# Performance work log

Measured on AMD Instinct MI355X. Metric: run time of the kernel, lower is better.

The kernel has to match this reference:

```python
import jax, jax.numpy as jnp
import numpy as np

PATCH = (2, 4, 4)
WIN = 4
SHIFT = 2
NLAYERS = 16  # depth=8 -> 8 (no-shift, shift) pairs interleaved
PD = 32       # patch_dim = 2*4*4
D_MAIN = 64   # patch_dim * 2
NHEAD = 2
HEAD_DIM = D_MAIN // NHEAD
FFN = 2
EPS = 1.1920929e-07  # torch.finfo(float32).eps (nn.RMSNorm default eps=None)


def rms_norm(x, w):
    return x * jax.lax.rsqrt(jnp.mean(x * x, axis=-1, keepdims=True) + EPS) * w


def _attn_mask(grid):
    # standard Swin shifted-window mask, built statically with numpy
    Dg, Hg, Wg = grid
    w, s = WIN, SHIFT
    img = np.zeros(grid, np.int32)
    cnt = 0
    sl = (slice(0, -w), slice(-w, -s), slice(-s, None))
    for a in sl:
        for b in sl:
            for c in sl:
                img[a, b, c] = cnt
                cnt += 1
    m = img.reshape(Dg // w, w, Hg // w, w, Wg // w, w)
    m = m.transpose(0, 2, 4, 1, 3, 5).reshape(-1, w ** 3)  # (nW, N)
    mask = np.where(m[:, None, :] != m[:, :, None], -100.0, 0.0).astype(np.float32)
    return jnp.asarray(mask)  # (nW, N, N)


def _window_partition(x, w):
    # (B, Dg, Hg, Wg, C) -> (B*nW, w^3, C)
    B, Dg, Hg, Wg, C = x.shape
    x = x.reshape(B, Dg // w, w, Hg // w, w, Wg // w, w, C)
    return x.transpose(0, 1, 3, 5, 2, 4, 6, 7).reshape(-1, w ** 3, C)


def _window_reverse(x, w, B, Dg, Hg, Wg):
    C = x.shape[-1]
    x = x.reshape(B, Dg // w, Hg // w, Wg // w, w, w, w, C)
    return x.transpose(0, 1, 4, 2, 5, 3, 6, 7).reshape(B, Dg, Hg, Wg, C)


def _swin_layer(x, grid, shift, mask, ln1, qkv_w, proj_w, proj_b, ln2, w1, b1, w2, b2):
    B, L, C = x.shape
    Dg, Hg, Wg = grid
    N = WIN ** 3
    shortcut = x
    h = rms_norm(x, ln1).reshape(B, Dg, Hg, Wg, C)
    if shift:
        h = jnp.roll(h, (-shift, -shift, -shift), axis=(1, 2, 3))
    hw = _window_partition(h, WIN)  # (Bw, N, C)
    Bw = hw.shape[0]
    qkv = (hw @ qkv_w).reshape(Bw, N, 3, NHEAD, HEAD_DIM)
    q, k, v = qkv[:, :, 0], qkv[:, :, 1], qkv[:, :, 2]  # (Bw, N, nh, hd)
    attn = jnp.einsum('bnhd,bmhd->bhnm', q, k) * (HEAD_DIM ** -0.5)
    if mask is not None:
        nW = mask.shape[0]
        attn = (attn.reshape(B, nW, NHEAD, N, N) + mask[None, :, None]).reshape(Bw, NHEAD, N, N)
    attn = jax.nn.softmax(attn, axis=-1)
    out = jnp.einsum('bhnm,bmhd->bnhd', attn, v).reshape(Bw, N, C)
    out = out @ proj_w + proj_b
    h = _window_reverse(out, WIN, B, Dg, Hg, Wg)
    if shift:
        h = jnp.roll(h, (shift, shift, shift), axis=(1, 2, 3))
    x = shortcut + h.reshape(B, L, C)
    h = rms_norm(x, ln2)
    h = jax.nn.gelu(h @ w1 + b1, approximate=False) @ w2 + b2
    return x + h


def setup_inputs() -> dict:
    key = jax.random.key(0)
    ks = jax.random.split(key, 10)
    def w(k, shape):
        return (jax.random.normal(k, shape, jnp.float32) * 0.02)
    B, D, H, W = 1, 64, 256, 256
    return {
        'x': jax.random.normal(ks[0], (B, 1, D, H, W), jnp.float32),
        'up_w': w(ks[1], (PD, D_MAIN)), 'up_b': jnp.zeros((D_MAIN,), jnp.float32),
        'ln1_w': jnp.ones((NLAYERS, D_MAIN), jnp.float32),
        'qkv_w': w(ks[2], (NLAYERS, D_MAIN, 3 * D_MAIN)),
        'proj_w': w(ks[3], (NLAYERS, D_MAIN, D_MAIN)),
        'proj_b': jnp.zeros((NLAYERS, D_MAIN), jnp.float32),
        'ln2_w': jnp.ones((NLAYERS, D_MAIN), jnp.float32),
        'mlp_w1': w(ks[4], (NLAYERS, D_MAIN, FFN * D_MAIN)),
        'mlp_b1': jnp.zeros((NLAYERS, FFN * D_MAIN), jnp.float32),
        'mlp_w2': w(ks[5], (NLAYERS, FFN * D_MAIN, D_MAIN)),
        'mlp_b2': jnp.zeros((NLAYERS, D_MAIN), jnp.float32),
        'down_p_w': w(ks[6], (D_MAIN, PD)), 'down_p_b': jnp.zeros((PD,), jnp.float32),
        'down_c_w': w(ks[7], (D_MAIN, PD)), 'down_c_b': jnp.zeros((PD,), jnp.float32),
    }


def reference(x, up_w, up_b, ln1_w, qkv_w, proj_w, proj_b, ln2_w,
              mlp_w1, mlp_b1, mlp_w2, mlp_b2, down_p_w, down_p_b, down_c_w, down_c_b):
    B, C, D, H, W = x.shape
    pd, ph, pw = PATCH
    Dg, Hg, Wg = D // pd, H // ph, W // pw
    L = Dg * Hg * Wg
    # unfoldNd (kernel == stride): non-overlapping patch extraction
    t = x.reshape(B, Dg, pd, Hg, ph, Wg, pw)
    t = t.transpose(0, 1, 3, 5, 2, 4, 6).reshape(B, L, PD)
    h = t @ up_w + up_b  # (B, L, 64)
    mask = _attn_mask((Dg, Hg, Wg))
    for i in range(NLAYERS):
        shift = SHIFT if (i % 2 == 1) else 0
        h = _swin_layer(h, (Dg, Hg, Wg), shift, mask if shift else None,
                        ln1_w[i], qkv_w[i], proj_w[i], proj_b[i], ln2_w[i],
                        mlp_w1[i], mlp_b1[i], mlp_w2[i], mlp_b2[i])
    p = h @ down_p_w + down_p_b
    c = h @ down_c_w + down_c_b
    def fold(t):
        t = t.reshape(B, Dg, Hg, Wg, pd, ph, pw)
        return t.transpose(0, 1, 4, 2, 5, 3, 6).reshape(B, 1, D, H, W)
    return (fold(p), fold(c))
```

## Files before the change

kernel.cpp:

```cpp
#include <hip/hip_runtime.h>
#include <hip/hip_bf16.h>


#define EPSV 1.1920929e-07f
#define QSW 196
#define HAW 72
#define HA_LO (64*72)
#define HTW 136
#define HT_LO (64*136)

typedef short short8 __attribute__((ext_vector_type(8)));
typedef float f32x4 __attribute__((ext_vector_type(4)));

#define MFMA3(d, ah_, al_, bh_, bl_)                                     \
    d = __builtin_amdgcn_mfma_f32_16x16x32_bf16(ah_, bh_, d, 0, 0, 0);   \
    d = __builtin_amdgcn_mfma_f32_16x16x32_bf16(ah_, bl_, d, 0, 0, 0);   \
    d = __builtin_amdgcn_mfma_f32_16x16x32_bf16(al_, bh_, d, 0, 0, 0);

__device__ __forceinline__ void split2(float v, short& hs, short& ls) {
    unsigned u = __float_as_uint(v);
    float hf = __uint_as_float(u & 0xFFFF0000u);
    float lf = v - hf;
    hs = (short)(u >> 16);
    ls = (short)(__float_as_uint(lf) >> 16);
}

__global__ __launch_bounds__(256) void k_embed(const float* __restrict__ x,
        const float* __restrict__ up_w, const float* __restrict__ up_b,
        float* __restrict__ h) {
    int t = blockIdx.x * 256 + threadIdx.x;
    int tok = t >> 2, seg = t & 3;
    int xg = tok & 63, yg = (tok >> 6) & 63, zg = tok >> 12;
    const float* xp = x + ((size_t)(zg * 2) * 256 + yg * 4) * 256 + xg * 4;
    float p[32];
    #pragma unroll
    for (int dz = 0; dz < 2; ++dz)
        #pragma unroll
        for (int dy = 0; dy < 4; ++dy) {
            float4 v = *reinterpret_cast<const float4*>(xp + ((size_t)dz * 256 + dy) * 256);
            int b = (dz * 4 + dy) * 4;
            p[b] = v.x; p[b + 1] = v.y; p[b + 2] = v.z; p[b + 3] = v.w;
        }
    float acc[16];
    #pragma unroll
    for (int j = 0; j < 16; ++j) acc[j] = up_b[seg * 16 + j];
    #pragma unroll
    for (int k = 0; k < 32; ++k) {
        float a = p[k];
        const float* wr = up_w + k * 64 + seg * 16;
        #pragma unroll
        for (int j = 0; j < 16; ++j) acc[j] = fmaf(a, wr[j], acc[j]);
    }
    float* op = h + (size_t)tok * 64 + seg * 16;
    #pragma unroll
    for (int j = 0; j < 16; ++j) op[j] = acc[j];
}

template <int SHIFTED>
__global__ __launch_bounds__(256, 2) void k_layer(float* __restrict__ h,
        const float* __restrict__ ln1, const float* __restrict__ qkvw,
        const float* __restrict__ projw, const float* __restrict__ projb,
        const float* __restrict__ ln2, const float* __restrict__ w1,
        const float* __restrict__ b1, const float* __restrict__ w2,
        const float* __restrict__ b2) {
    __shared__ __align__(16) unsigned short hA[2 * 64 * HAW];
    __shared__ __align__(16) float qs[64 * QSW];
    __shared__ int rid_s[64];

    float* hAf = (float*)hA;
    unsigned short* ht_hi = (unsigned short*)qs;
    unsigned short* ht_lo = (unsigned short*)qs + HT_LO;

    int w = blockIdx.x;
    int wx = w & 15, wy = (w >> 4) & 15, wz = w >> 8;
    int tid = threadIdx.x;
    int tok = tid >> 2, seg = tid & 3;
    int wv = tid >> 6, lane = tid & 63, lr = lane & 15, lg = lane >> 4;

    float v[16];
    int lidx;

    {
        int nz = tok >> 4, ny = (tok >> 2) & 3, nx = tok & 3;
        int gz = wz * 4 + nz, gy = wy * 4 + ny, gx = wx * 4 + nx;
        int sz, sy, sx;
        if (SHIFTED) { sz = (gz + 2) & 31; sy = (gy + 2) & 63; sx = (gx + 2) & 63; }
        else         { sz = gz; sy = gy; sx = gx; }
        lidx = (sz * 64 + sy) * 64 + sx;
        if (SHIFTED && seg == 0) {
            int rz = gz >= 30 ? 2 : (gz >= 28 ? 1 : 0);
            int ry = gy >= 62 ? 2 : (gy >= 60 ? 1 : 0);
            int rx = gx >= 62 ? 2 : (gx >= 60 ? 1 : 0);
            rid_s[tok] = rz * 9 + ry * 3 + rx;
        }
        const float* hp = h + (size_t)lidx * 64 + seg * 16;
        #pragma unroll
        for (int c = 0; c < 4; ++c) {
            float4 t4 = *reinterpret_cast<const float4*>(hp + c * 4);
            v[c * 4] = t4.x; v[c * 4 + 1] = t4.y; v[c * 4 + 2] = t4.z; v[c * 4 + 3] = t4.w;
        }
        float ss = 0.f;
        #pragma unroll
        for (int j = 0; j < 16; ++j) ss = fmaf(v[j], v[j], ss);
        ss += __shfl_xor(ss, 1);
        ss += __shfl_xor(ss, 2);
        float r = rsqrtf(ss * (1.0f / 64.0f) + EPSV);
        short8 sh[2], sl[2];
        #pragma unroll
        for (int j = 0; j < 16; ++j) {
            float nv = v[j] * r * ln1[seg * 16 + j];
            short hs, ls; split2(nv, hs, ls);
            sh[j >> 3][j & 7] = hs; sl[j >> 3][j & 7] = ls;
        }
        *reinterpret_cast<short8*>(&hA[tok * HAW + seg * 16])         = sh[0];
        *reinterpret_cast<short8*>(&hA[tok * HAW + seg * 16 + 8])     = sh[1];
        *reinterpret_cast<short8*>(&hA[HA_LO + tok * HAW + seg * 16])     = sl[0];
        *reinterpret_cast<short8*>(&hA[HA_LO + tok * HAW + seg * 16 + 8]) = sl[1];
    }
    __syncthreads();

    {
        short8 ah[4][2], al[4][2];
        #pragma unroll
        for (int mt = 0; mt < 4; ++mt)
            #pragma unroll
            for (int ks = 0; ks < 2; ++ks) {
                int off = (mt * 16 + lr) * HAW + ks * 32 + lg * 8;
                ah[mt][ks] = *reinterpret_cast<const short8*>(&hA[off]);
                al[mt][ks] = *reinterpret_cast<const short8*>(&hA[HA_LO + off]);
            }
        #pragma unroll
        for (int nt = 0; nt < 3; ++nt) {
            int c0 = wv * 48 + nt * 16;
            short8 bh[2], bl[2];
            #pragma unroll
            for (int ks = 0; ks < 2; ++ks) {
                const float* p = qkvw + (size_t)(ks * 32 + lg * 8) * 192 + c0 + lr;
                #pragma unroll
                for (int e = 0; e < 8; ++e) {
                    short hs, ls; split2(p[e * 192], hs, ls);
                    bh[ks][e] = hs; bl[ks][e] = ls;
                }
            }
            f32x4 acc[4];
            #pragma unroll
            for (int mt = 0; mt < 4; ++mt) acc[mt] = (f32x4)(0.f);
            #pragma unroll
            for (int mt = 0; mt < 4; ++mt)
                #pragma unroll
                for (int ks = 0; ks < 2; ++ks) {
                    MFMA3(acc[mt], ah[mt][ks], al[mt][ks], bh[ks], bl[ks]);
                }
            #pragma unroll
            for (int mt = 0; mt < 4; ++mt)
                #pragma unroll
                for (int j = 0; j < 4; ++j)
                    qs[(mt * 16 + lg * 4 + j) * QSW + c0 + lr] = acc[mt][j];
        }
    }
    __syncthreads();

    {
        int hh = tid >> 7, n = (tid >> 1) & 63, dh = tid & 1;
        int qo = hh * 32 + dh * 16;
        float q[16];
        #pragma unroll
        for (int c = 0; c < 4; ++c) {
            float4 t4 = *reinterpret_cast<const float4*>(&qs[n * QSW + qo + c * 4]);
            q[c * 4] = t4.x; q[c * 4 + 1] = t4.y; q[c * 4 + 2] = t4.z; q[c * 4 + 3] = t4.w;
        }
        float s[64];
        int myrid = SHIFTED ? rid_s[n] : 0;
        const float scale = 0.17677669529663687f;
        #pragma unroll
        for (int m = 0; m < 64; ++m) {
            float a = 0.f;
            #pragma unroll
            for (int c = 0; c < 4; ++c) {
                float4 kv = *reinterpret_cast<const float4*>(&qs[m * QSW + 64 + qo + c * 4]);
                a = fmaf(q[c * 4 + 0], kv.x, a);
                a = fmaf(q[c * 4 + 1], kv.y, a);
                a = fmaf(q[c * 4 + 2], kv.z, a);
                a = fmaf(q[c * 4 + 3], kv.w, a);
            }
            a += __shfl_xor(a, 1);
            a *= scale;
            if (SHIFTED && rid_s[m] != myrid) a -= 100.f;
            s[m] = a;
        }
        float mx = s[0];
        #pragma unroll
        for (int m = 1; m < 64; ++m) mx = fmaxf(mx, s[m]);
        float sum = 0.f;
        #pragma unroll
        for (int m = 0; m < 64; ++m) { float e = __expf(s[m] - mx); s[m] = e; sum += e; }
        float inv = 1.0f / sum;
        float o[16];
        #pragma unroll
        for (int j = 0; j < 16; ++j) o[j] = 0.f;
        #pragma unroll
        for (int m = 0; m < 64; ++m) {
            float p = s[m];
            #pragma unroll
            for (int c = 0; c < 4; ++c) {
                float4 vv = *reinterpret_cast<const float4*>(&qs[m * QSW + 128 + qo + c * 4]);
                o[c * 4 + 0] = fmaf(p, vv.x, o[c * 4 + 0]);
                o[c * 4 + 1] = fmaf(p, vv.y, o[c * 4 + 1]);
                o[c * 4 + 2] = fmaf(p, vv.z, o[c * 4 + 2]);
                o[c * 4 + 3] = fmaf(p, vv.w, o[c * 4 + 3]);
            }
        }
        short8 sh[2], sl[2];
        #pragma unroll
        for (int j = 0; j < 16; ++j) {
            short hs, ls; split2(o[j] * inv, hs, ls);
            sh[j >> 3][j & 7] = hs; sl[j >> 3][j & 7] = ls;
        }
        *reinterpret_cast<short8*>(&hA[n * HAW + qo])             = sh[0];
        *reinterpret_cast<short8*>(&hA[n * HAW + qo + 8])         = sh[1];
        *reinterpret_cast<short8*>(&hA[HA_LO + n * HAW + qo])     = sl[0];
        *reinterpret_cast<short8*>(&hA[HA_LO + n * HAW + qo + 8]) = sl[1];
    }
    __syncthreads();

    {
        short8 ah[4][2], al[4][2];
        #pragma unroll
        for (int mt = 0; mt < 4; ++mt)
            #pragma unroll
            for (int ks = 0; ks < 2; ++ks) {
                int off = (mt * 16 + lr) * HAW + ks * 32 + lg * 8;
                ah[mt][ks] = *reinterpret_cast<const short8*>(&hA[off]);
                al[mt][ks] = *reinterpret_cast<const short8*>(&hA[HA_LO + off]);
            }
        int c0 = wv * 16;
        short8 bh[2], bl[2];
        #pragma unroll
        for (int ks = 0; ks < 2; ++ks) {
            const float* p = projw + (size_t)(ks * 32 + lg * 8) * 64 + c0 + lr;
            #pragma unroll
            for (int e = 0; e < 8; ++e) {
                short hs, ls; split2(p[e * 64], hs, ls);
                bh[ks][e] = hs; bl[ks][e] = ls;
            }
        }
        f32x4 acc[4];
        #pragma unroll
        for (int mt = 0; mt < 4; ++mt) acc[mt] = (f32x4)(0.f);
        #pragma unroll
        for (int mt = 0; mt < 4; ++mt)
            #pragma unroll
            for (int ks = 0; ks < 2; ++ks) {
                MFMA3(acc[mt], ah[mt][ks], al[mt][ks], bh[ks], bl[ks]);
            }
        float pb = projb[c0 + lr];
        #pragma unroll
        for (int mt = 0; mt < 4; ++mt)
            #pragma unroll
            for (int j = 0; j < 4; ++j)
                qs[(mt * 16 + lg * 4 + j) * QSW + c0 + lr] = acc[mt][j] + pb;
    }
    __syncthreads();

    {
        #pragma unroll
        for (int j = 0; j < 16; ++j) v[j] += qs[tok * QSW + seg * 16 + j];
        float ss = 0.f;
        #pragma unroll
        for (int j = 0; j < 16; ++j) ss = fmaf(v[j], v[j], ss);
        ss += __shfl_xor(ss, 1);
        ss += __shfl_xor(ss, 2);
        float r = rsqrtf(ss * (1.0f / 64.0f) + EPSV);
        short8 sh[2], sl[2];
        #pragma unroll
        for (int j = 0; j < 16; ++j) {
            float nv = v[j] * r * ln2[seg * 16 + j];
            short hs, ls; split2(nv, hs, ls);
            sh[j >> 3][j & 7] = hs; sl[j >> 3][j & 7] = ls;
        }
        *reinterpret_cast<short8*>(&hA[tok * HAW + seg * 16])         = sh[0];
        *reinterpret_cast<short8*>(&hA[tok * HAW + seg * 16 + 8])     = sh[1];
        *reinterpret_cast<short8*>(&hA[HA_LO + tok * HAW + seg * 16])     = sl[0];
        *reinterpret_cast<short8*>(&hA[HA_LO + tok * HAW + seg * 16 + 8]) = sl[1];
    }
    __syncthreads();

    {
        short8 ah[4][2], al[4][2];
        #pragma unroll
        for (int mt = 0; mt < 4; ++mt)
            #pragma unroll
            for (int ks = 0; ks < 2; ++ks) {
                int off = (mt * 16 + lr) * HAW + ks * 32 + lg * 8;
                ah[mt][ks] = *reinterpret_cast<const short8*>(&hA[off]);
                al[mt][ks] = *reinterpret_cast<const short8*>(&hA[HA_LO + off]);
            }
        #pragma unroll
        for (int nt = 0; nt < 2; ++nt) {
            int c0 = wv * 32 + nt * 16;
            short8 bh[2], bl[2];
            #pragma unroll
            for (int ks = 0; ks < 2; ++ks) {
                const float* p = w1 + (size_t)(ks * 32 + lg * 8) * 128 + c0 + lr;
                #pragma unroll
                for (int e = 0; e < 8; ++e) {
                    short hs, ls; split2(p[e * 128], hs, ls);
                    bh[ks][e] = hs; bl[ks][e] = ls;
                }
            }
            f32x4 acc[4];
            #pragma unroll
            for (int mt = 0; mt < 4; ++mt) acc[mt] = (f32x4)(0.f);
            #pragma unroll
            for (int mt = 0; mt < 4; ++mt)
                #pragma unroll
                for (int ks = 0; ks < 2; ++ks) {
                    MFMA3(acc[mt], ah[mt][ks], al[mt][ks], bh[ks], bl[ks]);
                }
            float bb = b1[c0 + lr];
            #pragma unroll
            for (int mt = 0; mt < 4; ++mt)
                #pragma unroll
                for (int j = 0; j < 4; ++j) {
                    float u = acc[mt][j] + bb;
                    float g = 0.5f * u * (1.0f + erff(u * 0.70710678118654752f));
                    short hs, ls; split2(g, hs, ls);
                    int off = (mt * 16 + lg * 4 + j) * HTW + c0 + lr;
                    ht_hi[off] = (unsigned short)hs;
                    ht_lo[off] = (unsigned short)ls;
                }
        }
    }
    __syncthreads();

    {
        int c0 = wv * 16;
        f32x4 acc[4];
        #pragma unroll
        for (int mt = 0; mt < 4; ++mt) acc[mt] = (f32x4)(0.f);
        #pragma unroll
        for (int ks = 0; ks < 4; ++ks) {
            short8 bh, bl;
            const float* p = w2 + (size_t)(ks * 32 + lg * 8) * 64 + c0 + lr;
            #pragma unroll
            for (int e = 0; e < 8; ++e) {
                short hs, ls; split2(p[e * 64], hs, ls);
                bh[e] = hs; bl[e] = ls;
            }
            #pragma unroll
            for (int mt = 0; mt < 4; ++mt) {
                int off = (mt * 16 + lr) * HTW + ks * 32 + lg * 8;
                short8 ah = *reinterpret_cast<const short8*>(&ht_hi[off]);
                short8 al = *reinterpret_cast<const short8*>(&ht_lo[off]);
                MFMA3(acc[mt], ah, al, bh, bl);
            }
        }
        __syncthreads();
        float bb = b2[c0 + lr];
        #pragma unroll
        for (int mt = 0; mt < 4; ++mt)
            #pragma unroll
            for (int j = 0; j < 4; ++j)
                hAf[(mt * 16 + lg * 4 + j) * HAW + c0 + lr] = acc[mt][j] + bb;
    }
    __syncthreads();

    {
        float* op = h + (size_t)lidx * 64 + seg * 16;
        #pragma unroll
        for (int c = 0; c < 4; ++c) {
            float4 o4;
            o4.x = v[c * 4 + 0] + hAf[tok * HAW + seg * 16 + c * 4 + 0];
            o4.y = v[c * 4 + 1] + hAf[tok * HAW + seg * 16 + c * 4 + 1];
            o4.z = v[c * 4 + 2] + hAf[tok * HAW + seg * 16 + c * 4 + 2];
            o4.w = v[c * 4 + 3] + hAf[tok * HAW + seg * 16 + c * 4 + 3];
            *reinterpret_cast<float4*>(op + c * 4) = o4;
        }
    }
}

__global__ __launch_bounds__(256) void k_down(const float* __restrict__ h,
        const float* __restrict__ wp, const float* __restrict__ bp,
        const float* __restrict__ wc, const float* __restrict__ bc,
        float* __restrict__ out) {
    int t = blockIdx.x * 256 + threadIdx.x;
    int tok = t >> 1, pc = t & 1;
    const float* wsel = pc ? wc : wp;
    const float* bsel = pc ? bc : bp;
    float* obase = out + (size_t)pc * (64u * 256u * 256u);
    float hv[64];
    const float* hp = h + (size_t)tok * 64;
    #pragma unroll
    for (int j4 = 0; j4 < 16; ++j4) {
        float4 t4 = *reinterpret_cast<const float4*>(hp + j4 * 4);
        hv[j4 * 4] = t4.x; hv[j4 * 4 + 1] = t4.y; hv[j4 * 4 + 2] = t4.z; hv[j4 * 4 + 3] = t4.w;
    }
    float acc[32];
    #pragma unroll
    for (int j = 0; j < 32; ++j) acc[j] = bsel[j];
    #pragma unroll 4
    for (int k = 0; k < 64; ++k) {
        float a = hv[k];
        const float* wr = wsel + k * 32;
        #pragma unroll
        for (int j = 0; j < 32; ++j) acc[j] = fmaf(a, wr[j], acc[j]);
    }
    int xg = tok & 63, yg = (tok >> 6) & 63, zg = tok >> 12;
    float* op = obase + ((size_t)(zg * 2) * 256 + yg * 4) * 256 + xg * 4;
    #pragma unroll
    for (int dz = 0; dz < 2; ++dz)
        #pragma unroll
        for (int dy = 0; dy < 4; ++dy) {
            int b = (dz * 4 + dy) * 4;
            *reinterpret_cast<float4*>(op + ((size_t)dz * 256 + dy) * 256) =
                make_float4(acc[b], acc[b + 1], acc[b + 2], acc[b + 3]);
        }
}

extern "C" void kernel_launch(void* const* d_in, const int* in_sizes, int n_in,
                              void* d_out, int out_size, void* d_ws, size_t ws_size,
                              hipStream_t stream) {
    const float* x        = (const float*)d_in[0];
    const float* up_w     = (const float*)d_in[1];
    const float* up_b     = (const float*)d_in[2];
    const float* ln1_w    = (const float*)d_in[3];
    const float* qkv_w    = (const float*)d_in[4];
    const float* proj_w   = (const float*)d_in[5];
    const float* proj_b   = (const float*)d_in[6];
    const float* ln2_w    = (const float*)d_in[7];
    const float* mlp_w1   = (const float*)d_in[8];
    const float* mlp_b1   = (const float*)d_in[9];
    const float* mlp_w2   = (const float*)d_in[10];
    const float* mlp_b2   = (const float*)d_in[11];
    const float* down_p_w = (const float*)d_in[12];
    const float* down_p_b = (const float*)d_in[13];
    const float* down_c_w = (const float*)d_in[14];
    const float* down_c_b = (const float*)d_in[15];
    float* out = (float*)d_out;
    float* h   = (float*)d_ws;

    k_embed<<<2048, 256, 0, stream>>>(x, up_w, up_b, h);
    for (int i = 0; i < 16; ++i) {
        const float* a0 = ln1_w + i * 64;
        const float* a1 = qkv_w  + (size_t)i * 64 * 192;
        const float* a2 = proj_w + (size_t)i * 64 * 64;
        const float* a3 = proj_b + i * 64;
        const float* a4 = ln2_w + i * 64;
        const float* a5 = mlp_w1 + (size_t)i * 64 * 128;
        const float* a6 = mlp_b1 + i * 128;
        const float* a7 = mlp_w2 + (size_t)i * 128 * 64;
        const float* a8 = mlp_b2 + i * 64;
        if (i & 1) k_layer<1><<<2048, 256, 0, stream>>>(h, a0, a1, a2, a3, a4, a5, a6, a7, a8);
        else       k_layer<0><<<2048, 256, 0, stream>>>(h, a0, a1, a2, a3, a4, a5, a6, a7, a8);
    }
    k_down<<<1024, 256, 0, stream>>>(h, down_p_w, down_p_b, down_c_w, down_c_b, out);
}
```

Measured before the change: 1.856 ms.

## Pre-split weights into bf16 hi/lo MFMA fragment layout and restage down-projection

Adds a prologue kernel that splits all per-layer weight matrices once into bf16 hi/lo halves, stored in the exact per-lane MFMA B-fragment order. Each layer kernel then loads whole short8 fragments instead of doing eight strided fp32 gathers plus splits per fragment, in every block. The down-projection kernel is also rewritten so each block stages a row of tokens and both weight matrices in shared memory, computing both outputs per thread with float4 stores. This costs one extra launch and a workspace region at a fixed 32MB offset, which assumes the workspace is large enough.

```diff
diff --git a/kernel.cpp b/kernel.cpp
--- a/kernel.cpp
+++ b/kernel.cpp
@@ -9,6 +9,13 @@
 #define HTW 136
 #define HT_LO (64*136)
 
+#define LAYER_WSZ 32768
+#define WOFF_QKV  0
+#define WOFF_PROJ 12288
+#define WOFF_W1   16384
+#define WOFF_W2   24576
+#define WTOT      (16 * LAYER_WSZ)
+
 typedef short short8 __attribute__((ext_vector_type(8)));
 typedef float f32x4 __attribute__((ext_vector_type(4)));
 
@@ -23,6 +30,30 @@
     float lf = v - hf;
     hs = (short)(u >> 16);
     ls = (short)(__float_as_uint(lf) >> 16);
+}
+
+__global__ __launch_bounds__(256) void k_wsplit(const float* __restrict__ qkv_w,
+        const float* __restrict__ proj_w, const float* __restrict__ w1,
+        const float* __restrict__ w2, unsigned short* __restrict__ wsout) {
+    int t = blockIdx.x * 256 + threadIdx.x;
+    int layer = t >> 15;
+    int r = t & 32767;
+    const float* src; int ncols, idx, nks;
+    if (r < WOFF_PROJ)      { src = qkv_w  + (size_t)layer * 12288; ncols = 192; idx = r;             nks = 2; }
+    else if (r < WOFF_W1)   { src = proj_w + (size_t)layer * 4096;  ncols = 64;  idx = r - WOFF_PROJ; nks = 2; }
+    else if (r < WOFF_W2)   { src = w1     + (size_t)layer * 8192;  ncols = 128; idx = r - WOFF_W1;   nks = 2; }
+    else                    { src = w2     + (size_t)layer * 8192;  ncols = 64;  idx = r - WOFF_W2;   nks = 4; }
+    int e  = idx & 7;
+    int lr = (idx >> 3) & 15;
+    int lg = (idx >> 7) & 3;
+    int q  = idx >> 9;
+    int ks = q & (nks - 1);
+    int ct = q / nks;
+    int k = ks * 32 + lg * 8 + e;
+    int c = ct * 16 + lr;
+    short hs, ls; split2(src[k * ncols + c], hs, ls);
+    wsout[t]        = (unsigned short)hs;
+    wsout[WTOT + t] = (unsigned short)ls;
 }
 
 __global__ __launch_bounds__(256) void k_embed(const float* __restrict__ x,
@@ -58,11 +89,10 @@
 
 template <int SHIFTED>
 __global__ __launch_bounds__(256, 2) void k_layer(float* __restrict__ h,
-        const float* __restrict__ ln1, const float* __restrict__ qkvw,
-        const float* __restrict__ projw, const float* __restrict__ projb,
-        const float* __restrict__ ln2, const float* __restrict__ w1,
-        const float* __restrict__ b1, const float* __restrict__ w2,
-        const float* __restrict__ b2) {
+        const float* __restrict__ ln1,
+        const unsigned short* __restrict__ whi, const unsigned short* __restrict__ wlo,
+        const float* __restrict__ projb, const float* __restrict__ ln2,
+        const float* __restrict__ b1, const float* __restrict__ b2) {
     __shared__ __align__(16) unsigned short hA[2 * 64 * HAW];
     __shared__ __align__(16) float qs[64 * QSW];
     __shared__ int rid_s[64];
@@ -131,16 +161,14 @@
             }
         #pragma unroll
         for (int nt = 0; nt < 3; ++nt) {
-            int c0 = wv * 48 + nt * 16;
+            int ct = wv * 3 + nt;
+            int c0 = ct * 16;
             short8 bh[2], bl[2];
             #pragma unroll
             for (int ks = 0; ks < 2; ++ks) {
-                const float* p = qkvw + (size_t)(ks * 32 + lg * 8) * 192 + c0 + lr;
-                #pragma unroll
-                for (int e = 0; e < 8; ++e) {
-                    short hs, ls; split2(p[e * 192], hs, ls);
-                    bh[ks][e] = hs; bl[ks][e] = ls;
-                }
+                int fo = WOFF_QKV + ((ct * 2 + ks) * 4 + lg) * 128 + lr * 8;
+                bh[ks] = *reinterpret_cast<const short8*>(&whi[fo]);
+                bl[ks] = *reinterpret_cast<const short8*>(&wlo[fo]);
             }
             f32x4 acc[4];
             #pragma unroll
@@ -237,12 +265,9 @@
         short8 bh[2], bl[2];
         #pragma unroll
         for (int ks = 0; ks < 2; ++ks) {
-            const float* p = projw + (size_t)(ks * 32 + lg * 8) * 64 + c0 + lr;
-            #pragma unroll
-            for (int e = 0; e < 8; ++e) {
-                short hs, ls; split2(p[e * 64], hs, ls);
-                bh[ks][e] = hs; bl[ks][e] = ls;
-            }
+            int fo = WOFF_PROJ + ((wv * 2 + ks) * 4 + lg) * 128 + lr * 8;
+            bh[ks] = *reinterpret_cast<const short8*>(&whi[fo]);
+            bl[ks] = *reinterpret_cast<const short8*>(&wlo[fo]);
         }
         f32x4 acc[4];
         #pragma unroll
@@ -297,16 +322,14 @@
             }
         #pragma unroll
         for (int nt = 0; nt < 2; ++nt) {
-            int c0 = wv * 32 + nt * 16;
+            int ct = wv * 2 + nt;
+            int c0 = ct * 16;
             short8 bh[2], bl[2];
             #pragma unroll
             for (int ks = 0; ks < 2; ++ks) {
-                const float* p = w1 + (size_t)(ks * 32 + lg * 8) * 128 + c0 + lr;
-                #pragma unroll
-                for (int e = 0; e < 8; ++e) {
-                    short hs, ls; split2(p[e * 128], hs, ls);
-                    bh[ks][e] = hs; bl[ks][e] = ls;
-                }
+                int fo = WOFF_W1 + ((ct * 2 + ks) * 4 + lg) * 128 + lr * 8;
+                bh[ks] = *reinterpret_cast<const short8*>(&whi[fo]);
+                bl[ks] = *reinterpret_cast<const short8*>(&wlo[fo]);
             }
             f32x4 acc[4];
             #pragma unroll
@@ -340,13 +363,9 @@
         for (int mt = 0; mt < 4; ++mt) acc[mt] = (f32x4)(0.f);
         #pragma unroll
         for (int ks = 0; ks < 4; ++ks) {
-            short8 bh, bl;
-            const float* p = w2 + (size_t)(ks * 32 + lg * 8) * 64 + c0 + lr;
-            #pragma unroll
-            for (int e = 0; e < 8; ++e) {
-                short hs, ls; split2(p[e * 64], hs, ls);
-                bh[e] = hs; bl[e] = ls;
-            }
+            int fo = WOFF_W2 + ((wv * 4 + ks) * 4 + lg) * 128 + lr * 8;
+            short8 bh = *reinterpret_cast<const short8*>(&whi[fo]);
+            short8 bl = *reinterpret_cast<const short8*>(&wlo[fo]);
             #pragma unroll
             for (int mt = 0; mt < 4; ++mt) {
                 int off = (mt * 16 + lr) * HTW + ks * 32 + lg * 8;
@@ -383,37 +402,60 @@
         const float* __restrict__ wp, const float* __restrict__ bp,
         const float* __restrict__ wc, const float* __restrict__ bc,
         float* __restrict__ out) {
-    int t = blockIdx.x * 256 + threadIdx.x;
-    int tok = t >> 1, pc = t & 1;
-    const float* wsel = pc ? wc : wp;
-    const float* bsel = pc ? bc : bp;
-    float* obase = out + (size_t)pc * (64u * 256u * 256u);
+    __shared__ float hs_[64][68];
+    __shared__ float ws_[2][64][32];
+    int b = blockIdx.x;
+    int zg = b >> 6, yg = b & 63;
+    int tid = threadIdx.x;
+    const float* hp = h + (size_t)(zg * 64 + yg) * 64 * 64;
+    for (int i = tid; i < 1024; i += 256) {
+        float4 t4 = reinterpret_cast<const float4*>(hp)[i];
+        int tokx = i >> 4, c4 = (i & 15) * 4;
+        *reinterpret_cast<float4*>(&hs_[tokx][c4]) = t4;
+    }
+    for (int i = tid; i < 512; i += 256) {
+        reinterpret_cast<float4*>(&ws_[0][0][0])[i] = reinterpret_cast<const float4*>(wp)[i];
+        reinterpret_cast<float4*>(&ws_[1][0][0])[i] = reinterpret_cast<const float4*>(wc)[i];
+    }
+    __syncthreads();
+    int dc = tid >> 6, xg = tid & 63;
     float hv[64];
-    const float* hp = h + (size_t)tok * 64;
-    #pragma unroll
-    for (int j4 = 0; j4 < 16; ++j4) {
-        float4 t4 = *reinterpret_cast<const float4*>(hp + j4 * 4);
-        hv[j4 * 4] = t4.x; hv[j4 * 4 + 1] = t4.y; hv[j4 * 4 + 2] = t4.z; hv[j4 * 4 + 3] = t4.w;
-    }
-    float acc[32];
-    #pragma unroll
-    for (int j = 0; j < 32; ++j) acc[j] = bsel[j];
-    #pragma unroll 4
+    #pragma unroll
+    for (int j = 0; j < 16; ++j) {
+        float4 t4 = *reinterpret_cast<const float4*>(&hs_[xg][j * 4]);
+        hv[j * 4] = t4.x; hv[j * 4 + 1] = t4.y; hv[j * 4 + 2] = t4.z; hv[j * 4 + 3] = t4.w;
+    }
+    float4 acc[2][2];
+    #pragma unroll
+    for (int pc = 0; pc < 2; ++pc) {
+        const float* bsel = pc ? bc : bp;
+        #pragma unroll
+        for (int ci = 0; ci < 2; ++ci)
+            acc[pc][ci] = *reinterpret_cast<const float4*>(bsel + (dc + ci * 4) * 4);
+    }
+    #pragma unroll 8
     for (int k = 0; k < 64; ++k) {
         float a = hv[k];
-        const float* wr = wsel + k * 32;
-        #pragma unroll
-        for (int j = 0; j < 32; ++j) acc[j] = fmaf(a, wr[j], acc[j]);
-    }
-    int xg = tok & 63, yg = (tok >> 6) & 63, zg = tok >> 12;
-    float* op = obase + ((size_t)(zg * 2) * 256 + yg * 4) * 256 + xg * 4;
-    #pragma unroll
-    for (int dz = 0; dz < 2; ++dz)
-        #pragma unroll
-        for (int dy = 0; dy < 4; ++dy) {
-            int b = (dz * 4 + dy) * 4;
-            *reinterpret_cast<float4*>(op + ((size_t)dz * 256 + dy) * 256) =
-                make_float4(acc[b], acc[b + 1], acc[b + 2], acc[b + 3]);
+        #pragma unroll
+        for (int pc = 0; pc < 2; ++pc)
+            #pragma unroll
+            for (int ci = 0; ci < 2; ++ci) {
+                float4 w4 = *reinterpret_cast<const float4*>(&ws_[pc][k][(dc + ci * 4) * 4]);
+                acc[pc][ci].x = fmaf(a, w4.x, acc[pc][ci].x);
+                acc[pc][ci].y = fmaf(a, w4.y, acc[pc][ci].y);
+                acc[pc][ci].z = fmaf(a, w4.z, acc[pc][ci].z);
+                acc[pc][ci].w = fmaf(a, w4.w, acc[pc][ci].w);
+            }
+    }
+    #pragma unroll
+    for (int pc = 0; pc < 2; ++pc)
+        #pragma unroll
+        for (int ci = 0; ci < 2; ++ci) {
+            int cb = dc + ci * 4;
+            int dz = cb >> 2, dy = cb & 3;
+            float* op = out + (size_t)pc * (64u * 256u * 256u)
+                      + ((size_t)(zg * 2 + dz) * 256 + (yg * 4 + dy)) * 256 + xg * 4;
+            *reinterpret_cast<float4*>(op) = acc[pc][ci];
         }
 }
 
@@ -438,20 +480,17 @@
     const float* down_c_b = (const float*)d_in[15];
     float* out = (float*)d_out;
     float* h   = (float*)d_ws;
-
+    unsigned short* wsw = (unsigned short*)((char*)d_ws + (size_t)32 * 1024 * 1024);
+
+    k_wsplit<<<2048, 256, 0, stream>>>(qkv_w, proj_w, mlp_w1, mlp_w2, wsw);
     k_embed<<<2048, 256, 0, stream>>>(x, up_w, up_b, h);
     for (int i = 0; i < 16; ++i) {
-        const float* a0 = ln1_w + i * 64;
-        const float* a1 = qkv_w  + (size_t)i * 64 * 192;
-        const float* a2 = proj_w + (size_t)i * 64 * 64;
-        const float* a3 = proj_b + i * 64;
-        const float* a4 = ln2_w + i * 64;
-        const float* a5 = mlp_w1 + (size_t)i * 64 * 128;
-        const float* a6 = mlp_b1 + i * 128;
-        const float* a7 = mlp_w2 + (size_t)i * 128 * 64;
-        const float* a8 = mlp_b2 + i * 64;
-        if (i & 1) k_layer<1><<<2048, 256, 0, stream>>>(h, a0, a1, a2, a3, a4, a5, a6, a7, a8);
-        else       k_layer<0><<<2048, 256, 0, stream>>>(h, a0, a1, a2, a3, a4, a5, a6, a7, a8);
-    }
-    k_down<<<1024, 256, 0, stream>>>(h, down_p_w, down_p_b, down_c_w, down_c_b, out);
-}
+        const unsigned short* whi = wsw + (size_t)i * LAYER_WSZ;
+        const unsigned short* wlo = wsw + WTOT + (size_t)i * LAYER_WSZ;
+        if (i & 1) k_layer<1><<<2048, 256, 0, stream>>>(h, ln1_w + i * 64, whi, wlo,
+                proj_b + i * 64, ln2_w + i * 64, mlp_b1 + i * 128, mlp_b2 + i * 64);
+        else       k_layer<0><<<2048, 256, 0, stream>>>(h, ln1_w + i * 64, whi, wlo,
+                proj_b + i * 64, ln2_w + i * 64, mlp_b1 + i * 128, mlp_b2 + i * 64);
+    }
+    k_down<<<2048, 256, 0, stream>>>(h, down_p_w, down_p_b, down_c_w, down_c_b, out);
+}
```

After: 1.697 ms. -8.6%, faster.
